# Performance work log

Measured on AMD Instinct MI355X. Metric: run time of the kernel, lower is better.

The kernel has to match this reference:

```python
import jax, jax.numpy as jnp
import numpy as np

B, D, E, H, OUT = 4096, 1024, 8, 4096, 1024


def setup_inputs() -> dict:
    key = jax.random.key(0)
    ks = jax.random.split(key, 8)
    s_in = 1.0 / np.sqrt(D)
    s_h = 1.0 / np.sqrt(H)
    return {
        "x": jax.random.normal(ks[0], (B, D), dtype=jnp.float32),
        "Wg": jax.random.uniform(ks[1], (D, E), minval=-s_in, maxval=s_in, dtype=jnp.float32),
        "bg": jnp.zeros((E,), dtype=jnp.float32),
        "W1": jax.random.uniform(ks[2], (E, D, H), minval=-s_in, maxval=s_in, dtype=jnp.float32),
        "b1": jnp.zeros((E, H), dtype=jnp.float32),
        "W2": jax.random.uniform(ks[3], (E, H, OUT), minval=-s_h, maxval=s_h, dtype=jnp.float32),
        "b2": jnp.zeros((E, OUT), dtype=jnp.float32),
        "w_bal": jnp.float32(0.01),
    }


def reference(x, Wg, bg, W1, b1, W2, b2, w_bal):
    # Gating: softmax then top-1 (== argmax of logits)
    gate_logits = x @ Wg + bg                      # [B, E]
    assign = jnp.argmax(gate_logits, axis=1)       # [B] top-1 expert
    onehot = jax.nn.one_hot(assign, E, dtype=x.dtype)  # [B, E] dispatch mask

    # Dense dispatch: run every expert MLP, combine by one-hot (top-1 select).
    # Original returns raw expert output (no gate-prob scaling).
    h = jax.nn.relu(jnp.einsum("bd,edh->ebh", x, W1) + b1[:, None, :])  # [E, B, H]
    y = jnp.einsum("ebh,eho->ebo", h, W2) + b2[:, None, :]              # [E, B, OUT]
    output = jnp.einsum("ebo,be->bo", y, onehot)                        # [B, OUT]

    # Load-balance loss on per-expert token counts
    loads = onehot.sum(axis=0)                     # [E]
    balance_loss = jnp.sum((loads - loads.mean()) ** 2) / E
    return output, balance_loss * w_bal
```

## Files before the change

### kernel.cpp

```cpp
#include <hip/hip_runtime.h>
#include <hip/hip_bf16.h>

typedef unsigned short u16;
typedef __attribute__((ext_vector_type(8))) short bf16x8;
typedef __attribute__((ext_vector_type(4))) float f32x4;

#define BTOK 4096
#define DDIM 1024
#define NEXP 8
#define HDIM 4096
#define ODIM 1024
#define MAXTILES 40
#define MAXROWS (MAXTILES * 128)

__device__ __forceinline__ u16 f2bf(float f) {
  unsigned u = __float_as_uint(f);
  return (u16)((u + 0x7FFFu + ((u >> 16) & 1u)) >> 16);
}

__device__ __forceinline__ void gload16(const void* g, void* l) {
  __builtin_amdgcn_global_load_lds(
      (const __attribute__((address_space(1))) void*)g,
      (__attribute__((address_space(3))) void*)l, 16, 0, 0);
}

__global__ __launch_bounds__(256) void init_kernel(int* __restrict__ ctrl,
                                                   int* __restrict__ rowmap) {
  int i = blockIdx.x * 256 + threadIdx.x;
  if (i < 1024)
    ctrl[i] = 0;
  else
    rowmap[i - 1024] = -1;
}

__global__ __launch_bounds__(256) void gate_kernel(
    const float* __restrict__ x, const float* __restrict__ Wg,
    const float* __restrict__ bg, int* __restrict__ assign,
    int* __restrict__ counts) {
  int wave = threadIdx.x >> 6;
  int lane = threadIdx.x & 63;
  int b = blockIdx.x * 4 + wave;
  const float* xr = x + (size_t)b * DDIM;
  double acc[NEXP];
#pragma unroll
  for (int e = 0; e < NEXP; ++e) acc[e] = 0.0;
  for (int d = lane; d < DDIM; d += 64) {
    float xv = xr[d];
    const float4* wrow = (const float4*)(Wg + d * NEXP);
    float4 w0 = wrow[0], w1 = wrow[1];
    acc[0] += (double)xv * (double)w0.x;
    acc[1] += (double)xv * (double)w0.y;
    acc[2] += (double)xv * (double)w0.z;
    acc[3] += (double)xv * (double)w0.w;
    acc[4] += (double)xv * (double)w1.x;
    acc[5] += (double)xv * (double)w1.y;
    acc[6] += (double)xv * (double)w1.z;
    acc[7] += (double)xv * (double)w1.w;
  }
#pragma unroll
  for (int e = 0; e < NEXP; ++e) {
    double v = acc[e];
#pragma unroll
    for (int off = 32; off > 0; off >>= 1) v += __shfl_xor(v, off);
    acc[e] = v;
  }
  if (lane == 0) {
    int best = 0;
    double bv = acc[0] + (double)bg[0];
#pragma unroll
    for (int e = 1; e < NEXP; ++e) {
      double v = acc[e] + (double)bg[e];
      if (v > bv) { bv = v; best = e; }
    }
    assign[b] = best;
    atomicAdd(&counts[best], 1);
  }
}

__global__ void setup_kernel(const int* __restrict__ counts,
                             const float* __restrict__ wbal,
                             int* __restrict__ offp, int* __restrict__ tile_e,
                             int* __restrict__ tile_m, int* __restrict__ meta,
                             float* __restrict__ loss_out) {
  if (threadIdx.x != 0 || blockIdx.x != 0) return;
  int off = 0, nt = 0;
  for (int e = 0; e < NEXP; ++e) {
    offp[e] = off;
    int pc = (counts[e] + 127) & ~127;
    for (int t = 0; t < (pc >> 7); ++t) {
      tile_e[nt] = e;
      tile_m[nt] = off + t * 128;
      ++nt;
    }
    off += pc;
  }
  offp[NEXP] = off;
  meta[0] = nt;
  float mean = (float)BTOK / (float)NEXP;
  float s = 0.f;
  for (int e = 0; e < NEXP; ++e) {
    float d = (float)counts[e] - mean;
    s += d * d;
  }
  loss_out[0] = s / (float)NEXP * wbal[0];
}

__global__ __launch_bounds__(256) void gather_kernel(
    const float* __restrict__ x, const int* __restrict__ assign,
    const int* __restrict__ offp, int* __restrict__ fill,
    int* __restrict__ rowmap, u16* __restrict__ xg) {
  int b = blockIdx.x;
  __shared__ int srow;
  if (threadIdx.x == 0) {
    int e = assign[b];
    int pos = atomicAdd(&fill[e], 1);
    int row = offp[e] + pos;
    rowmap[row] = b;
    srow = row;
  }
  __syncthreads();
  int row = srow;
  float4 v = *(const float4*)(x + (size_t)b * DDIM + threadIdx.x * 4);
  ushort4 o;
  o.x = f2bf(v.x);
  o.y = f2bf(v.y);
  o.z = f2bf(v.z);
  o.w = f2bf(v.w);
  *(ushort4*)(xg + (size_t)row * DDIM + threadIdx.x * 4) = o;
}

__global__ __launch_bounds__(256) void transpose_conv(
    const float* __restrict__ W, u16* __restrict__ wt, int inN,
    size_t estrideIn, int k0, int n0, int KR, int NC) {
  const int e = blockIdx.z;
  const int kb = blockIdx.x * 64, nb = blockIdx.y * 64;
  __shared__ float lds[64][68];
  const float* src = W + (size_t)e * estrideIn + (size_t)k0 * inN + n0;
  const int t = threadIdx.x;
  const int rr = t >> 4, cc = (t & 15) * 4;
#pragma unroll
  for (int p = 0; p < 4; ++p) {
    float4 v = *(const float4*)(src + (size_t)(kb + rr + p * 16) * inN + nb + cc);
    *(float4*)&lds[rr + p * 16][cc] = v;
  }
  __syncthreads();
  const int n = t & 63, kg = (t >> 6) * 16;
  u16 tmp[16];
#pragma unroll
  for (int i = 0; i < 16; ++i) tmp[i] = f2bf(lds[kg + i][n]);
  u16* dst = wt + ((size_t)e * NC + nb + n) * KR + kb + kg;
  *(float4*)dst = *(float4*)&tmp[0];
  *(float4*)(dst + 8) = *(float4*)&tmp[8];
}

template <int MODE>
__global__ __launch_bounds__(256) void moe_gemm(
    const u16* __restrict__ A, int lda, const u16* __restrict__ BT, int ldb,
    int nbRows, const float* __restrict__ bias, int biasLd, int cOff,
    const int* __restrict__ tile_e, const int* __restrict__ tile_m,
    const int* __restrict__ meta, u16* __restrict__ Hout, int ldh,
    float* __restrict__ P, size_t pStride, int nkt) {
  const int nx = gridDim.x;
  const int nwg = nx * gridDim.y;
  const int orig = blockIdx.y * nx + blockIdx.x;
  const int q = nwg >> 3;
  const int wg = (orig & 7) * q + (orig >> 3);
  const int bx = wg % nx, by = wg / nx;
  if (bx >= meta[0]) return;
  const int e = tile_e[bx];
  const int m0 = tile_m[bx];
  const int n0 = by * 128;
  const int kOff = blockIdx.z * nkt * 32;

  __shared__ __align__(16) u16 lds[2 * 8192];

  const int tid = threadIdx.x;
  const int lane = tid & 63;
  const int wave = tid >> 6;
  const int wr = wave >> 1, wc = wave & 1;
  const int fr = lane & 15;
  const int kqr = lane >> 4;

  const int r0 = tid >> 2, k0 = (tid & 3) ^ ((r0 >> 1) & 3);
  const int r1 = (tid + 256) >> 2, k1 = ((tid + 256) & 3) ^ ((r1 >> 1) & 3);
  const u16* aS0 = A + (size_t)(m0 + r0) * lda + kOff + k0 * 8;
  const u16* aS1 = A + (size_t)(m0 + r1) * lda + kOff + k1 * 8;
  const u16* bPan = BT + ((size_t)e * nbRows + n0) * ldb + kOff;
  const u16* bS0 = bPan + (size_t)r0 * ldb + k0 * 8;
  const u16* bS1 = bPan + (size_t)r1 * ldb + k1 * 8;
  const int dst0 = (tid & ~63) * 8;
  const int dst1 = dst0 + 2048;

  int aOff[4], bOff[4];
#pragma unroll
  for (int i = 0; i < 4; ++i) {
    int r = wr * 64 + i * 16 + fr;
    aOff[i] = (r * 4 + (kqr ^ ((r >> 1) & 3))) * 8;
    int c = wc * 64 + i * 16 + fr;
    bOff[i] = (c * 4 + (kqr ^ ((c >> 1) & 3))) * 8;
  }

  f32x4 acc[4][4];
#pragma unroll
  for (int i = 0; i < 4; ++i)
#pragma unroll
    for (int j = 0; j < 4; ++j)
#pragma unroll
      for (int r = 0; r < 4; ++r) acc[i][j][r] = 0.f;

  auto stage = [&](int c, int kt) {
    const int ko = kt * 32;
    u16* base = lds + c * 8192;
    gload16(aS0 + ko, base + dst0);
    gload16(aS1 + ko, base + dst1);
    gload16(bS0 + ko, base + 4096 + dst0);
    gload16(bS1 + ko, base + 4096 + dst1);
  };
  auto compute = [&](int c) {
    const u16* base = lds + c * 8192;
    bf16x8 af[4], bfr[4];
#pragma unroll
    for (int i = 0; i < 4; ++i) {
      af[i] = *(const bf16x8*)(base + aOff[i]);
      bfr[i] = *(const bf16x8*)(base + 4096 + bOff[i]);
    }
#pragma unroll
    for (int i = 0; i < 4; ++i)
#pragma unroll
      for (int j = 0; j < 4; ++j)
        acc[i][j] = __builtin_amdgcn_mfma_f32_16x16x32_bf16(af[i], bfr[j],
                                                            acc[i][j], 0, 0, 0);
  };

  stage(0, 0);
  __syncthreads();
  int cur = 0;
#pragma unroll 1
  for (int kt = 0; kt < nkt - 1; ++kt) {
    stage(cur ^ 1, kt + 1);
    compute(cur);
    __syncthreads();
    cur ^= 1;
  }
  compute(cur);

  if constexpr (MODE == 0) {
#pragma unroll
    for (int i = 0; i < 4; ++i) {
      int rbase = m0 + wr * 64 + i * 16 + (lane >> 4) * 4;
#pragma unroll
      for (int j = 0; j < 4; ++j) {
        int col = n0 + wc * 64 + j * 16 + fr;
        float bv = bias[e * biasLd + cOff + col];
#pragma unroll
        for (int r = 0; r < 4; ++r) {
          float v = acc[i][j][r] + bv;
          v = v > 0.f ? v : 0.f;
          Hout[(size_t)(rbase + r) * ldh + col] = f2bf(v);
        }
      }
    }
  } else {
    float* Pp = P + blockIdx.z * pStride;
#pragma unroll
    for (int i = 0; i < 4; ++i) {
      int rbase = m0 + wr * 64 + i * 16 + (lane >> 4) * 4;
#pragma unroll
      for (int j = 0; j < 4; ++j) {
        int col = n0 + wc * 64 + j * 16 + fr;
#pragma unroll
        for (int r = 0; r < 4; ++r) {
          size_t idx = (size_t)(rbase + r) * ODIM + col;
          if constexpr (MODE == 1)
            Pp[idx] = acc[i][j][r];
          else
            Pp[idx] += acc[i][j][r];
        }
      }
    }
  }
}

__global__ __launch_bounds__(256) void reduce_kernel(
    const float* __restrict__ P, size_t pStride, const int* __restrict__ rowmap,
    const int* __restrict__ tile_e, const int* __restrict__ tile_m,
    const int* __restrict__ meta, const float* __restrict__ b2,
    float* __restrict__ out) {
  if ((int)blockIdx.x >= meta[0]) return;
  const int e = tile_e[blockIdx.x];
  const int m0 = tile_m[blockIdx.x];
  const int c0 = blockIdx.y * 128;
#pragma unroll 1
  for (int it = 0; it < 16; ++it) {
    int idx = it * 256 + threadIdx.x;
    int r = idx >> 5, cq = idx & 31;
    int row = m0 + r;
    int tok = rowmap[row];
    if (tok < 0) continue;
    int c = c0 + cq * 4;
    float4 a = *(const float4*)(P + (size_t)row * ODIM + c);
    float4 b = *(const float4*)(P + pStride + (size_t)row * ODIM + c);
    float4 bb = *(const float4*)(b2 + (size_t)e * ODIM + c);
    float4 o;
    o.x = a.x + b.x + bb.x;
    o.y = a.y + b.y + bb.y;
    o.z = a.z + b.z + bb.z;
    o.w = a.w + b.w + bb.w;
    *(float4*)(out + (size_t)tok * ODIM + c) = o;
  }
}

extern "C" void kernel_launch(void* const* d_in, const int* in_sizes, int n_in,
                              void* d_out, int out_size, void* d_ws,
                              size_t ws_size, hipStream_t stream) {
  const float* x = (const float*)d_in[0];
  const float* Wg = (const float*)d_in[1];
  const float* bg = (const float*)d_in[2];
  const float* W1 = (const float*)d_in[3];
  const float* b1 = (const float*)d_in[4];
  const float* W2 = (const float*)d_in[5];
  const float* b2 = (const float*)d_in[6];
  const float* wbal = (const float*)d_in[7];
  float* out = (float*)d_out;

  char* ws = (char*)d_ws;
  int* counts = (int*)(ws + 0);
  int* fill = (int*)(ws + 64);
  int* offp = (int*)(ws + 128);
  int* meta = (int*)(ws + 192);
  int* tile_e = (int*)(ws + 256);
  int* tile_m = (int*)(ws + 512);
  int* assign = (int*)(ws + 4096);
  int* rowmap = (int*)(ws + 20480);
  u16* xg = (u16*)(ws + 65536);

  const size_t hOff = 65536 + (size_t)MAXROWS * DDIM * 2;
  auto need = [&](size_t hc) {
    return hOff + (size_t)MAXROWS * hc * 2
           + (size_t)NEXP * hc * DDIM * 2
           + (size_t)NEXP * ODIM * hc * 2
           + 2 * (size_t)MAXROWS * ODIM * 4;
  };
  size_t HC = 4096;
  if (ws_size < need(4096)) HC = (ws_size >= need(2048)) ? 2048 : 1024;

  u16* h = (u16*)(ws + hOff);
  u16* wt1 = (u16*)((char*)h + (size_t)MAXROWS * HC * 2);
  u16* wt2 = (u16*)((char*)wt1 + (size_t)NEXP * HC * DDIM * 2);
  float* P = (float*)((char*)wt2 + (size_t)NEXP * ODIM * HC * 2);
  const size_t pStride = (size_t)MAXROWS * ODIM;

  init_kernel<<<24, 256, 0, stream>>>((int*)ws, rowmap);
  gate_kernel<<<BTOK / 4, 256, 0, stream>>>(x, Wg, bg, assign, counts);
  setup_kernel<<<1, 64, 0, stream>>>(counts, wbal, offp, tile_e, tile_m, meta,
                                     out + (size_t)BTOK * ODIM);
  gather_kernel<<<BTOK, 256, 0, stream>>>(x, assign, offp, fill, rowmap, xg);

  const int nch = HDIM / (int)HC;
  for (int c = 0; c < nch; ++c) {
    transpose_conv<<<dim3(DDIM / 64, HC / 64, NEXP), 256, 0, stream>>>(
        W1, wt1, HDIM, (size_t)DDIM * HDIM, 0, c * (int)HC, DDIM, (int)HC);
    moe_gemm<0><<<dim3(MAXTILES, HC / 128, 1), 256, 0, stream>>>(
        xg, DDIM, wt1, DDIM, (int)HC, b1, HDIM, c * (int)HC, tile_e, tile_m,
        meta, h, (int)HC, nullptr, 0, DDIM / 32);
    transpose_conv<<<dim3(HC / 64, ODIM / 64, NEXP), 256, 0, stream>>>(
        W2, wt2, ODIM, (size_t)HDIM * ODIM, c * (int)HC, 0, (int)HC, ODIM);
    if (c == 0)
      moe_gemm<1><<<dim3(MAXTILES, ODIM / 128, 2), 256, 0, stream>>>(
          h, (int)HC, wt2, (int)HC, ODIM, nullptr, 0, 0, tile_e, tile_m, meta,
          nullptr, 0, P, pStride, (int)HC / 64);
    else
      moe_gemm<2><<<dim3(MAXTILES, ODIM / 128, 2), 256, 0, stream>>>(
          h, (int)HC, wt2, (int)HC, ODIM, nullptr, 0, 0, tile_e, tile_m, meta,
          nullptr, 0, P, pStride, (int)HC / 64);
  }
  reduce_kernel<<<dim3(MAXTILES, ODIM / 128), 256, 0, stream>>>(
      P, pStride, rowmap, tile_e, tile_m, meta, b2, out);
}
```

Measured before the change: 359.9 us.

## Fuse weight fp32-to-bf16 conversion into GEMM B-tile loads, drop transpose kernels

Removes the separate transpose_conv passes that converted W1/W2 to transposed bf16 in the workspace. The GEMMs now read fp32 weights directly with per-thread strided column loads, convert to bf16 in registers and write them swizzled into LDS, with the global load issued before compute and the LDS write after it. This also drops the chunked HC loop, so there is one launch per GEMM, and workspace offsets become hardcoded. The cost is uncoalesced-looking strided fp32 loads (each thread walks rows of width LDN, though neighbouring threads read neighbouring columns), double the weight bytes fetched per tile, and more register pressure. Launch bounds now request 3 blocks per SM.

```diff
diff --git a/kernel.cpp b/kernel.cpp
--- a/kernel.cpp
+++ b/kernel.cpp
@@ -16,6 +16,12 @@
 __device__ __forceinline__ u16 f2bf(float f) {
   unsigned u = __float_as_uint(f);
   return (u16)((u + 0x7FFFu + ((u >> 16) & 1u)) >> 16);
+}
+__device__ __forceinline__ u16 cvt_bf(float f) {
+  __hip_bfloat16 h = __float2bfloat16(f);
+  u16 r;
+  __builtin_memcpy(&r, &h, 2);
+  return r;
 }
 
 __device__ __forceinline__ void gload16(const void* g, void* l) {
@@ -129,37 +135,12 @@
   *(ushort4*)(xg + (size_t)row * DDIM + threadIdx.x * 4) = o;
 }
 
-__global__ __launch_bounds__(256) void transpose_conv(
-    const float* __restrict__ W, u16* __restrict__ wt, int inN,
-    size_t estrideIn, int k0, int n0, int KR, int NC) {
-  const int e = blockIdx.z;
-  const int kb = blockIdx.x * 64, nb = blockIdx.y * 64;
-  __shared__ float lds[64][68];
-  const float* src = W + (size_t)e * estrideIn + (size_t)k0 * inN + n0;
-  const int t = threadIdx.x;
-  const int rr = t >> 4, cc = (t & 15) * 4;
-#pragma unroll
-  for (int p = 0; p < 4; ++p) {
-    float4 v = *(const float4*)(src + (size_t)(kb + rr + p * 16) * inN + nb + cc);
-    *(float4*)&lds[rr + p * 16][cc] = v;
-  }
-  __syncthreads();
-  const int n = t & 63, kg = (t >> 6) * 16;
-  u16 tmp[16];
-#pragma unroll
-  for (int i = 0; i < 16; ++i) tmp[i] = f2bf(lds[kg + i][n]);
-  u16* dst = wt + ((size_t)e * NC + nb + n) * KR + kb + kg;
-  *(float4*)dst = *(float4*)&tmp[0];
-  *(float4*)(dst + 8) = *(float4*)&tmp[8];
-}
-
-template <int MODE>
-__global__ __launch_bounds__(256) void moe_gemm(
-    const u16* __restrict__ A, int lda, const u16* __restrict__ BT, int ldb,
-    int nbRows, const float* __restrict__ bias, int biasLd, int cOff,
-    const int* __restrict__ tile_e, const int* __restrict__ tile_m,
-    const int* __restrict__ meta, u16* __restrict__ Hout, int ldh,
-    float* __restrict__ P, size_t pStride, int nkt) {
+template <int MODE, int LDA, int LDN>
+__global__ __launch_bounds__(256, 3) void moe_gemm(
+    const u16* __restrict__ A, const float* __restrict__ W, size_t eStride,
+    const float* __restrict__ bias, const int* __restrict__ tile_e,
+    const int* __restrict__ tile_m, const int* __restrict__ meta,
+    u16* __restrict__ Hout, float* __restrict__ P, size_t pStride, int nkt) {
   const int nx = gridDim.x;
   const int nwg = nx * gridDim.y;
   const int orig = blockIdx.y * nx + blockIdx.x;
@@ -183,13 +164,16 @@
 
   const int r0 = tid >> 2, k0 = (tid & 3) ^ ((r0 >> 1) & 3);
   const int r1 = (tid + 256) >> 2, k1 = ((tid + 256) & 3) ^ ((r1 >> 1) & 3);
-  const u16* aS0 = A + (size_t)(m0 + r0) * lda + kOff + k0 * 8;
-  const u16* aS1 = A + (size_t)(m0 + r1) * lda + kOff + k1 * 8;
-  const u16* bPan = BT + ((size_t)e * nbRows + n0) * ldb + kOff;
-  const u16* bS0 = bPan + (size_t)r0 * ldb + k0 * 8;
-  const u16* bS1 = bPan + (size_t)r1 * ldb + k1 * 8;
+  const u16* aS0 = A + (size_t)(m0 + r0) * LDA + kOff + k0 * 8;
+  const u16* aS1 = A + (size_t)(m0 + r1) * LDA + kOff + k1 * 8;
   const int dst0 = (tid & ~63) * 8;
   const int dst1 = dst0 + 2048;
+
+  const int bc = tid & 127;
+  const int bq0 = tid >> 7;
+  const float* bRow = W + (size_t)e * eStride + (size_t)kOff * LDN + n0 + bc;
+  const int bu0 = (bc * 4 + (bq0 ^ ((bc >> 1) & 3))) * 8;
+  const int bu1 = (bc * 4 + ((bq0 + 2) ^ ((bc >> 1) & 3))) * 8;
 
   int aOff[4], bOff[4];
 #pragma unroll
@@ -208,13 +192,29 @@
 #pragma unroll
       for (int r = 0; r < 4; ++r) acc[i][j][r] = 0.f;
 
-  auto stage = [&](int c, int kt) {
+  float fb[16];
+  auto loadB = [&](int kt) {
+    const float* p = bRow + (size_t)kt * 32 * LDN;
+#pragma unroll
+    for (int i = 0; i < 8; ++i) fb[i] = p[(size_t)(bq0 * 8 + i) * LDN];
+#pragma unroll
+    for (int i = 0; i < 8; ++i) fb[8 + i] = p[(size_t)((bq0 + 2) * 8 + i) * LDN];
+  };
+  auto writeB = [&](int c) {
+    u16* ldsB = lds + c * 8192 + 4096;
+    alignas(16) u16 tA[8], tB[8];
+#pragma unroll
+    for (int i = 0; i < 8; ++i) tA[i] = cvt_bf(fb[i]);
+#pragma unroll
+    for (int i = 0; i < 8; ++i) tB[i] = cvt_bf(fb[8 + i]);
+    *(bf16x8*)&ldsB[bu0] = *(const bf16x8*)tA;
+    *(bf16x8*)&ldsB[bu1] = *(const bf16x8*)tB;
+  };
+  auto stageA = [&](int c, int kt) {
     const int ko = kt * 32;
     u16* base = lds + c * 8192;
     gload16(aS0 + ko, base + dst0);
     gload16(aS1 + ko, base + dst1);
-    gload16(bS0 + ko, base + 4096 + dst0);
-    gload16(bS1 + ko, base + 4096 + dst1);
   };
   auto compute = [&](int c) {
     const u16* base = lds + c * 8192;
@@ -232,13 +232,17 @@
                                                             acc[i][j], 0, 0, 0);
   };
 
-  stage(0, 0);
+  loadB(0);
+  stageA(0, 0);
+  writeB(0);
   __syncthreads();
   int cur = 0;
 #pragma unroll 1
   for (int kt = 0; kt < nkt - 1; ++kt) {
-    stage(cur ^ 1, kt + 1);
+    loadB(kt + 1);
+    stageA(cur ^ 1, kt + 1);
     compute(cur);
+    writeB(cur ^ 1);
     __syncthreads();
     cur ^= 1;
   }
@@ -251,12 +255,12 @@
 #pragma unroll
       for (int j = 0; j < 4; ++j) {
         int col = n0 + wc * 64 + j * 16 + fr;
-        float bv = bias[e * biasLd + cOff + col];
+        float bv = bias[e * LDN + col];
 #pragma unroll
         for (int r = 0; r < 4; ++r) {
           float v = acc[i][j][r] + bv;
           v = v > 0.f ? v : 0.f;
-          Hout[(size_t)(rbase + r) * ldh + col] = f2bf(v);
+          Hout[(size_t)(rbase + r) * LDN + col] = f2bf(v);
         }
       }
     }
@@ -269,13 +273,8 @@
       for (int j = 0; j < 4; ++j) {
         int col = n0 + wc * 64 + j * 16 + fr;
 #pragma unroll
-        for (int r = 0; r < 4; ++r) {
-          size_t idx = (size_t)(rbase + r) * ODIM + col;
-          if constexpr (MODE == 1)
-            Pp[idx] = acc[i][j][r];
-          else
-            Pp[idx] += acc[i][j][r];
-        }
+        for (int r = 0; r < 4; ++r)
+          Pp[(size_t)(rbase + r) * ODIM + col] = acc[i][j][r];
       }
     }
   }
@@ -333,21 +332,8 @@
   int* assign = (int*)(ws + 4096);
   int* rowmap = (int*)(ws + 20480);
   u16* xg = (u16*)(ws + 65536);
-
-  const size_t hOff = 65536 + (size_t)MAXROWS * DDIM * 2;
-  auto need = [&](size_t hc) {
-    return hOff + (size_t)MAXROWS * hc * 2
-           + (size_t)NEXP * hc * DDIM * 2
-           + (size_t)NEXP * ODIM * hc * 2
-           + 2 * (size_t)MAXROWS * ODIM * 4;
-  };
-  size_t HC = 4096;
-  if (ws_size < need(4096)) HC = (ws_size >= need(2048)) ? 2048 : 1024;
-
-  u16* h = (u16*)(ws + hOff);
-  u16* wt1 = (u16*)((char*)h + (size_t)MAXROWS * HC * 2);
-  u16* wt2 = (u16*)((char*)wt1 + (size_t)NEXP * HC * DDIM * 2);
-  float* P = (float*)((char*)wt2 + (size_t)NEXP * ODIM * HC * 2);
+  u16* h = (u16*)(ws + 10551296);
+  float* P = (float*)(ws + 52494336);
   const size_t pStride = (size_t)MAXROWS * ODIM;
 
   init_kernel<<<24, 256, 0, stream>>>((int*)ws, rowmap);
@@ -356,24 +342,13 @@
                                      out + (size_t)BTOK * ODIM);
   gather_kernel<<<BTOK, 256, 0, stream>>>(x, assign, offp, fill, rowmap, xg);
 
-  const int nch = HDIM / (int)HC;
-  for (int c = 0; c < nch; ++c) {
-    transpose_conv<<<dim3(DDIM / 64, HC / 64, NEXP), 256, 0, stream>>>(
-        W1, wt1, HDIM, (size_t)DDIM * HDIM, 0, c * (int)HC, DDIM, (int)HC);
-    moe_gemm<0><<<dim3(MAXTILES, HC / 128, 1), 256, 0, stream>>>(
-        xg, DDIM, wt1, DDIM, (int)HC, b1, HDIM, c * (int)HC, tile_e, tile_m,
-        meta, h, (int)HC, nullptr, 0, DDIM / 32);
-    transpose_conv<<<dim3(HC / 64, ODIM / 64, NEXP), 256, 0, stream>>>(
-        W2, wt2, ODIM, (size_t)HDIM * ODIM, c * (int)HC, 0, (int)HC, ODIM);
-    if (c == 0)
-      moe_gemm<1><<<dim3(MAXTILES, ODIM / 128, 2), 256, 0, stream>>>(
-          h, (int)HC, wt2, (int)HC, ODIM, nullptr, 0, 0, tile_e, tile_m, meta,
-          nullptr, 0, P, pStride, (int)HC / 64);
-    else
-      moe_gemm<2><<<dim3(MAXTILES, ODIM / 128, 2), 256, 0, stream>>>(
-          h, (int)HC, wt2, (int)HC, ODIM, nullptr, 0, 0, tile_e, tile_m, meta,
-          nullptr, 0, P, pStride, (int)HC / 64);
-  }
+  moe_gemm<0, DDIM, HDIM><<<dim3(MAXTILES, HDIM / 128, 1), 256, 0, stream>>>(
+      xg, W1, (size_t)DDIM * HDIM, b1, tile_e, tile_m, meta, h, nullptr, 0,
+      DDIM / 32);
+  moe_gemm<1, HDIM, ODIM><<<dim3(MAXTILES, ODIM / 128, 2), 256, 0, stream>>>(
+      h, W2, (size_t)HDIM * ODIM, nullptr, tile_e, tile_m, meta, nullptr, P,
+      pStride, HDIM / 64);
+
   reduce_kernel<<<dim3(MAXTILES, ODIM / 128), 256, 0, stream>>>(
       P, pStride, rowmap, tile_e, tile_m, meta, b2, out);
 }
```

Result: faster. 327.8 us (-8.9%).

## Fuse weight transposes into gather and GEMM1 launches, drop HC chunking

Applied to the files above, without the earlier changes.

Merges the token gather with the W1 transpose/convert into one launch, and the first expert GEMM with the W2 transpose into another, so independent work shares a grid and fewer kernel launches occur. Removes the hidden-dim chunk loop and uses fixed workspace offsets, with each transpose block handling four 64-column subtiles. The GEMM main loop replaces __syncthreads with an explicit vmcnt wait plus raw barriers and raises wave priority around the MFMA block. Hardcoded offsets assume a large workspace, and the fallback to smaller HC chunks is gone.

```diff
diff --git a/kernel.cpp b/kernel.cpp
--- a/kernel.cpp
+++ b/kernel.cpp
@@ -16,6 +16,12 @@
 __device__ __forceinline__ u16 f2bf(float f) {
   unsigned u = __float_as_uint(f);
   return (u16)((u + 0x7FFFu + ((u >> 16) & 1u)) >> 16);
+}
+__device__ __forceinline__ u16 cvt_bf(float f) {
+  __hip_bfloat16 h = __float2bfloat16(f);
+  u16 r;
+  __builtin_memcpy(&r, &h, 2);
+  return r;
 }
 
 __device__ __forceinline__ void gload16(const void* g, void* l) {
@@ -105,74 +111,80 @@
   loss_out[0] = s / (float)NEXP * wbal[0];
 }
 
-__global__ __launch_bounds__(256) void gather_kernel(
+__device__ __forceinline__ void transpose_chunk(const float* __restrict__ W,
+                                                u16* __restrict__ wt, int K,
+                                                int N, int chunk,
+                                                float (*lds)[68]) {
+  const int t = threadIdx.x;
+  const int e = chunk >> 8;
+  const int r = chunk & 255;
+  const int nK = K >> 6;
+  const int kb = (r & (nK - 1)) * 64;
+  const int nb0 = (r / nK) * 256;
+  const float* src = W + (size_t)e * K * N;
+  const int rr = t >> 4, cc = (t & 15) * 4;
+  const int n = t & 63, kg = (t >> 6) * 16;
+#pragma unroll 1
+  for (int s = 0; s < 4; ++s) {
+    const int nb = nb0 + s * 64;
+#pragma unroll
+    for (int p = 0; p < 4; ++p) {
+      float4 v =
+          *(const float4*)(src + (size_t)(kb + rr + p * 16) * N + nb + cc);
+      *(float4*)&lds[rr + p * 16][cc] = v;
+    }
+    __syncthreads();
+    alignas(16) u16 tmp[16];
+#pragma unroll
+    for (int i = 0; i < 16; ++i) tmp[i] = cvt_bf(lds[kg + i][n]);
+    u16* dst = wt + ((size_t)e * N + nb + n) * K + kb + kg;
+    *(float4*)dst = *(float4*)&tmp[0];
+    *(float4*)(dst + 8) = *(float4*)&tmp[8];
+    __syncthreads();
+  }
+}
+
+__global__ __launch_bounds__(256, 4) void fused_gather_t1(
     const float* __restrict__ x, const int* __restrict__ assign,
     const int* __restrict__ offp, int* __restrict__ fill,
-    int* __restrict__ rowmap, u16* __restrict__ xg) {
-  int b = blockIdx.x;
-  __shared__ int srow;
-  if (threadIdx.x == 0) {
-    int e = assign[b];
-    int pos = atomicAdd(&fill[e], 1);
-    int row = offp[e] + pos;
-    rowmap[row] = b;
-    srow = row;
-  }
-  __syncthreads();
-  int row = srow;
-  float4 v = *(const float4*)(x + (size_t)b * DDIM + threadIdx.x * 4);
-  ushort4 o;
-  o.x = f2bf(v.x);
-  o.y = f2bf(v.y);
-  o.z = f2bf(v.z);
-  o.w = f2bf(v.w);
-  *(ushort4*)(xg + (size_t)row * DDIM + threadIdx.x * 4) = o;
-}
-
-__global__ __launch_bounds__(256) void transpose_conv(
-    const float* __restrict__ W, u16* __restrict__ wt, int inN,
-    size_t estrideIn, int k0, int n0, int KR, int NC) {
-  const int e = blockIdx.z;
-  const int kb = blockIdx.x * 64, nb = blockIdx.y * 64;
-  __shared__ float lds[64][68];
-  const float* src = W + (size_t)e * estrideIn + (size_t)k0 * inN + n0;
-  const int t = threadIdx.x;
-  const int rr = t >> 4, cc = (t & 15) * 4;
-#pragma unroll
-  for (int p = 0; p < 4; ++p) {
-    float4 v = *(const float4*)(src + (size_t)(kb + rr + p * 16) * inN + nb + cc);
-    *(float4*)&lds[rr + p * 16][cc] = v;
-  }
-  __syncthreads();
-  const int n = t & 63, kg = (t >> 6) * 16;
-  u16 tmp[16];
-#pragma unroll
-  for (int i = 0; i < 16; ++i) tmp[i] = f2bf(lds[kg + i][n]);
-  u16* dst = wt + ((size_t)e * NC + nb + n) * KR + kb + kg;
-  *(float4*)dst = *(float4*)&tmp[0];
-  *(float4*)(dst + 8) = *(float4*)&tmp[8];
+    int* __restrict__ rowmap, u16* __restrict__ xg,
+    const float* __restrict__ W1, u16* __restrict__ wt1) {
+  __shared__ __align__(16) float tl[64][68];
+  const int id = blockIdx.x;
+  if (id < BTOK) {
+    __shared__ int srow;
+    if (threadIdx.x == 0) {
+      int e = assign[id];
+      int pos = atomicAdd(&fill[e], 1);
+      int row = offp[e] + pos;
+      rowmap[row] = id;
+      srow = row;
+    }
+    __syncthreads();
+    int row = srow;
+    float4 v = *(const float4*)(x + (size_t)id * DDIM + threadIdx.x * 4);
+    ushort4 o;
+    o.x = f2bf(v.x);
+    o.y = f2bf(v.y);
+    o.z = f2bf(v.z);
+    o.w = f2bf(v.w);
+    *(ushort4*)(xg + (size_t)row * DDIM + threadIdx.x * 4) = o;
+  } else {
+    transpose_chunk(W1, wt1, DDIM, HDIM, id - BTOK, tl);
+  }
 }
 
 template <int MODE>
-__global__ __launch_bounds__(256) void moe_gemm(
-    const u16* __restrict__ A, int lda, const u16* __restrict__ BT, int ldb,
-    int nbRows, const float* __restrict__ bias, int biasLd, int cOff,
-    const int* __restrict__ tile_e, const int* __restrict__ tile_m,
-    const int* __restrict__ meta, u16* __restrict__ Hout, int ldh,
+__device__ __forceinline__ void gemm_core(
+    u16* lds, int bx, int by, int bz, const u16* __restrict__ A, int lda,
+    const u16* __restrict__ BT, int ldb, int nbRows,
+    const float* __restrict__ bias, const int* __restrict__ tile_e,
+    const int* __restrict__ tile_m, u16* __restrict__ Hout, int ldn,
     float* __restrict__ P, size_t pStride, int nkt) {
-  const int nx = gridDim.x;
-  const int nwg = nx * gridDim.y;
-  const int orig = blockIdx.y * nx + blockIdx.x;
-  const int q = nwg >> 3;
-  const int wg = (orig & 7) * q + (orig >> 3);
-  const int bx = wg % nx, by = wg / nx;
-  if (bx >= meta[0]) return;
   const int e = tile_e[bx];
   const int m0 = tile_m[bx];
   const int n0 = by * 128;
-  const int kOff = blockIdx.z * nkt * 32;
-
-  __shared__ __align__(16) u16 lds[2 * 8192];
+  const int kOff = bz * nkt * 32;
 
   const int tid = threadIdx.x;
   const int lane = tid & 63;
@@ -224,24 +236,34 @@
       af[i] = *(const bf16x8*)(base + aOff[i]);
       bfr[i] = *(const bf16x8*)(base + 4096 + bOff[i]);
     }
+    __builtin_amdgcn_s_setprio(1);
 #pragma unroll
     for (int i = 0; i < 4; ++i)
 #pragma unroll
       for (int j = 0; j < 4; ++j)
         acc[i][j] = __builtin_amdgcn_mfma_f32_16x16x32_bf16(af[i], bfr[j],
                                                             acc[i][j], 0, 0, 0);
+    __builtin_amdgcn_s_setprio(0);
   };
 
   stage(0, 0);
-  __syncthreads();
   int cur = 0;
 #pragma unroll 1
   for (int kt = 0; kt < nkt - 1; ++kt) {
     stage(cur ^ 1, kt + 1);
+    asm volatile("s_waitcnt vmcnt(4)" ::: "memory");
+    __builtin_amdgcn_sched_barrier(0);
+    __builtin_amdgcn_s_barrier();
+    __builtin_amdgcn_sched_barrier(0);
     compute(cur);
-    __syncthreads();
+    __builtin_amdgcn_sched_barrier(0);
+    __builtin_amdgcn_s_barrier();
     cur ^= 1;
   }
+  asm volatile("s_waitcnt vmcnt(0)" ::: "memory");
+  __builtin_amdgcn_sched_barrier(0);
+  __builtin_amdgcn_s_barrier();
+  __builtin_amdgcn_sched_barrier(0);
   compute(cur);
 
   if constexpr (MODE == 0) {
@@ -251,17 +273,17 @@
 #pragma unroll
       for (int j = 0; j < 4; ++j) {
         int col = n0 + wc * 64 + j * 16 + fr;
-        float bv = bias[e * biasLd + cOff + col];
+        float bv = bias[e * ldn + col];
 #pragma unroll
         for (int r = 0; r < 4; ++r) {
           float v = acc[i][j][r] + bv;
           v = v > 0.f ? v : 0.f;
-          Hout[(size_t)(rbase + r) * ldh + col] = f2bf(v);
+          Hout[(size_t)(rbase + r) * ldn + col] = f2bf(v);
         }
       }
     }
   } else {
-    float* Pp = P + blockIdx.z * pStride;
+    float* Pp = P + bz * pStride;
 #pragma unroll
     for (int i = 0; i < 4; ++i) {
       int rbase = m0 + wr * 64 + i * 16 + (lane >> 4) * 4;
@@ -269,16 +291,42 @@
       for (int j = 0; j < 4; ++j) {
         int col = n0 + wc * 64 + j * 16 + fr;
 #pragma unroll
-        for (int r = 0; r < 4; ++r) {
-          size_t idx = (size_t)(rbase + r) * ODIM + col;
-          if constexpr (MODE == 1)
-            Pp[idx] = acc[i][j][r];
-          else
-            Pp[idx] += acc[i][j][r];
-        }
+        for (int r = 0; r < 4; ++r)
+          Pp[(size_t)(rbase + r) * ODIM + col] = acc[i][j][r];
       }
     }
   }
+}
+
+__global__ __launch_bounds__(256, 4) void fused_g1_t2(
+    const u16* __restrict__ xg, const u16* __restrict__ wt1,
+    const float* __restrict__ b1, const float* __restrict__ W2,
+    u16* __restrict__ wt2, u16* __restrict__ h, const int* __restrict__ tile_e,
+    const int* __restrict__ tile_m, const int* __restrict__ meta) {
+  __shared__ __align__(16) char smem[32768];
+  const int id = blockIdx.x;
+  if (id < 1280) {
+    const int wg = (id & 7) * 160 + (id >> 3);
+    const int bx = wg % MAXTILES, by = wg / MAXTILES;
+    if (bx >= meta[0]) return;
+    gemm_core<0>((u16*)smem, bx, by, 0, xg, DDIM, wt1, DDIM, HDIM, b1, tile_e,
+                 tile_m, h, HDIM, nullptr, 0, DDIM / 32);
+  } else {
+    transpose_chunk(W2, wt2, HDIM, ODIM, id - 1280, (float(*)[68])smem);
+  }
+}
+
+__global__ __launch_bounds__(256, 4) void moe_gemm2(
+    const u16* __restrict__ h, const u16* __restrict__ wt2,
+    const int* __restrict__ tile_e, const int* __restrict__ tile_m,
+    const int* __restrict__ meta, float* __restrict__ P, size_t pStride) {
+  __shared__ __align__(16) u16 lds[2 * 8192];
+  const int orig = blockIdx.y * MAXTILES + blockIdx.x;
+  const int wg = (orig & 7) * 40 + (orig >> 3);
+  const int bx = wg % MAXTILES, by = wg / MAXTILES;
+  if (bx >= meta[0]) return;
+  gemm_core<1>(lds, bx, by, blockIdx.z, h, HDIM, wt2, HDIM, ODIM, nullptr,
+               tile_e, tile_m, nullptr, 0, P, pStride, (HDIM / 2) / 32);
 }
 
 __global__ __launch_bounds__(256) void reduce_kernel(
@@ -333,47 +381,22 @@
   int* assign = (int*)(ws + 4096);
   int* rowmap = (int*)(ws + 20480);
   u16* xg = (u16*)(ws + 65536);
-
-  const size_t hOff = 65536 + (size_t)MAXROWS * DDIM * 2;
-  auto need = [&](size_t hc) {
-    return hOff + (size_t)MAXROWS * hc * 2
-           + (size_t)NEXP * hc * DDIM * 2
-           + (size_t)NEXP * ODIM * hc * 2
-           + 2 * (size_t)MAXROWS * ODIM * 4;
-  };
-  size_t HC = 4096;
-  if (ws_size < need(4096)) HC = (ws_size >= need(2048)) ? 2048 : 1024;
-
-  u16* h = (u16*)(ws + hOff);
-  u16* wt1 = (u16*)((char*)h + (size_t)MAXROWS * HC * 2);
-  u16* wt2 = (u16*)((char*)wt1 + (size_t)NEXP * HC * DDIM * 2);
-  float* P = (float*)((char*)wt2 + (size_t)NEXP * ODIM * HC * 2);
+  u16* h = (u16*)(ws + 10551296);
+  float* P = (float*)(ws + 52494336);
+  u16* wt1 = (u16*)(ws + 94437376);
+  u16* wt2 = (u16*)(ws + 161546240);
   const size_t pStride = (size_t)MAXROWS * ODIM;
 
   init_kernel<<<24, 256, 0, stream>>>((int*)ws, rowmap);
   gate_kernel<<<BTOK / 4, 256, 0, stream>>>(x, Wg, bg, assign, counts);
   setup_kernel<<<1, 64, 0, stream>>>(counts, wbal, offp, tile_e, tile_m, meta,
                                      out + (size_t)BTOK * ODIM);
-  gather_kernel<<<BTOK, 256, 0, stream>>>(x, assign, offp, fill, rowmap, xg);
-
-  const int nch = HDIM / (int)HC;
-  for (int c = 0; c < nch; ++c) {
-    transpose_conv<<<dim3(DDIM / 64, HC / 64, NEXP), 256, 0, stream>>>(
-        W1, wt1, HDIM, (size_t)DDIM * HDIM, 0, c * (int)HC, DDIM, (int)HC);
-    moe_gemm<0><<<dim3(MAXTILES, HC / 128, 1), 256, 0, stream>>>(
-        xg, DDIM, wt1, DDIM, (int)HC, b1, HDIM, c * (int)HC, tile_e, tile_m,
-        meta, h, (int)HC, nullptr, 0, DDIM / 32);
-    transpose_conv<<<dim3(HC / 64, ODIM / 64, NEXP), 256, 0, stream>>>(
-        W2, wt2, ODIM, (size_t)HDIM * ODIM, c * (int)HC, 0, (int)HC, ODIM);
-    if (c == 0)
-      moe_gemm<1><<<dim3(MAXTILES, ODIM / 128, 2), 256, 0, stream>>>(
-          h, (int)HC, wt2, (int)HC, ODIM, nullptr, 0, 0, tile_e, tile_m, meta,
-          nullptr, 0, P, pStride, (int)HC / 64);
-    else
-      moe_gemm<2><<<dim3(MAXTILES, ODIM / 128, 2), 256, 0, stream>>>(
-          h, (int)HC, wt2, (int)HC, ODIM, nullptr, 0, 0, tile_e, tile_m, meta,
-          nullptr, 0, P, pStride, (int)HC / 64);
-  }
+  fused_gather_t1<<<BTOK + 2048, 256, 0, stream>>>(x, assign, offp, fill,
+                                                   rowmap, xg, W1, wt1);
+  fused_g1_t2<<<1280 + 2048, 256, 0, stream>>>(xg, wt1, b1, W2, wt2, h, tile_e,
+                                               tile_m, meta);
+  moe_gemm2<<<dim3(MAXTILES, ODIM / 128, 2), 256, 0, stream>>>(
+      h, wt2, tile_e, tile_m, meta, P, pStride);
   reduce_kernel<<<dim3(MAXTILES, ODIM / 128), 256, 0, stream>>>(
       P, pStride, rowmap, tile_e, tile_m, meta, b2, out);
 }
```

Result: no change. 356.7 us (-0.9%).
